# Optimization experiments

Measured on AMD Instinct MI355X. Metric: run time of the kernel, lower is better.

## Reference

```python
import jax, jax.numpy as jnp
import numpy as np

N, E = 100000, 1600000
IN, HID, HEADS, OUT = 128, 16, 8, 40
NEG_SLOPE = 0.2


def setup_inputs() -> dict:
    key = jax.random.key(0)
    ks = jax.random.split(key, 10)
    glorot = lambda k, shape, fan: (jax.random.normal(k, shape, jnp.float32) / np.float32(np.sqrt(fan)))
    return {
        "x": jax.random.normal(ks[0], (N, IN), jnp.float32),
        "edge_index": jax.random.randint(ks[1], (2, E), 0, N, dtype=jnp.int64),
        "W1": glorot(ks[2], (IN, HEADS * HID), IN),
        "att_src1": glorot(ks[3], (HEADS, HID), HID),
        "att_dst1": glorot(ks[4], (HEADS, HID), HID),
        "b1": jnp.zeros((HEADS * HID,), jnp.float32),
        "W2": glorot(ks[5], (HEADS * HID, OUT), HEADS * HID),
        "att_src2": glorot(ks[6], (1, OUT), OUT),
        "att_dst2": glorot(ks[7], (1, OUT), OUT),
        "b2": jnp.zeros((OUT,), jnp.float32),
    }


def gat_conv(x, W, a_src, a_dst, b, src, dst, n, heads, ch, concat):
    # x: [n, in], W: [in, heads*ch]
    h = (x @ W).reshape(n, heads, ch)                      # [n, H, C]
    e_s = jnp.einsum("nhc,hc->nh", h, a_src)               # per-node src logits
    e_d = jnp.einsum("nhc,hc->nh", h, a_dst)               # per-node dst logits
    alpha = jax.nn.leaky_relu(e_s[src] + e_d[dst], NEG_SLOPE)  # [E, H]
    # numerically stable softmax over incoming edges of each dst node
    m = jax.lax.stop_gradient(jax.ops.segment_max(alpha, dst, num_segments=n))
    ex = jnp.exp(alpha - m[dst])
    denom = jax.ops.segment_sum(ex, dst, num_segments=n)
    a = ex / (denom[dst] + 1e-16)                          # [E, H]
    out = jax.ops.segment_sum(h[src] * a[:, :, None], dst, num_segments=n)  # [n, H, C]
    out = out.reshape(n, heads * ch) if concat else out.mean(axis=1)
    return out + b


def reference(x, edge_index, W1, att_src1, att_dst1, b1, W2, att_src2, att_dst2, b2):
    n = x.shape[0]
    loops = jnp.arange(n, dtype=edge_index.dtype)
    src = jnp.concatenate([edge_index[0], loops])  # add_self_loops (PyG default)
    dst = jnp.concatenate([edge_index[1], loops])
    h1 = jax.nn.relu(gat_conv(x, W1, att_src1, att_dst1, b1, src, dst, n, HEADS, HID, True))
    # F.dropout(training=False) is identity in inference
    h2 = gat_conv(h1, W2, att_src2, att_dst2, b2, src, dst, n, 1, OUT, False)
    return jax.nn.log_softmax(h2, axis=1)
```

## Files before the change

### kernel.cpp

```cpp
#include <hip/hip_runtime.h>
#include <hip/hip_fp16.h>
#include <math.h>

#define NN 100000
#define EE 1600000
#define ET (EE + NN)
#define BWN 64
#define NBUCK 1563
#define ACHUNK 4096
#define NAB 416
#define MAXS 1792

typedef _Float16 f16x8 __attribute__((ext_vector_type(8)));
typedef float f32x4 __attribute__((ext_vector_type(4)));
typedef float f32x2 __attribute__((ext_vector_type(2)));

__device__ __forceinline__ float lrelu(float x) { return x > 0.f ? x : 0.2f * x; }

__global__ void k_w1pack(const float* __restrict__ W1, __half* __restrict__ w1p) {
    int idx = blockIdx.x * 256 + threadIdx.x;
    int j = idx & 7, lane = (idx >> 3) & 63, k0 = (idx >> 9) & 3;
    int ct = (idx >> 11) & 7, plane = idx >> 14;
    int k = k0 * 32 + (lane >> 4) * 8 + j;
    int c = ct * 16 + (lane & 15);
    float w = W1[k * 128 + c];
    _Float16 wh = (_Float16)w;
    _Float16 v = plane ? (_Float16)(w - (float)wh) : wh;
    w1p[idx] = *(__half*)&v;
}

__global__ __launch_bounds__(256) void k_gemm1(
        const float* __restrict__ x, const __half* __restrict__ w1p,
        const float* __restrict__ as1, const float* __restrict__ ad1,
        unsigned* __restrict__ h1b, float* __restrict__ es1, float* __restrict__ ed1) {
    int tid = threadIdx.x;
    int w = tid >> 6, lane = tid & 63;
    int rb = blockIdx.x * 64 + w * 16;
    int l15 = lane & 15, rg = lane >> 4;

    int arow = rb + l15;
    bool aok = arow < NN;
    const float4* x4 = (const float4*)x;
    f16x8 ah[4], ar[4];
    #pragma unroll
    for (int k0 = 0; k0 < 4; ++k0) {
        float4 p0 = make_float4(0.f, 0.f, 0.f, 0.f), p1 = p0;
        if (aok) {
            int fi = arow * 32 + k0 * 8 + rg * 2;
            p0 = x4[fi];
            p1 = x4[fi + 1];
        }
        float pv[8] = {p0.x, p0.y, p0.z, p0.w, p1.x, p1.y, p1.z, p1.w};
        #pragma unroll
        for (int j = 0; j < 8; ++j) {
            _Float16 h = (_Float16)pv[j];
            ah[k0][j] = h;
            ar[k0][j] = (_Float16)(pv[j] - (float)h);
        }
    }

    const f16x8* w1f = (const f16x8*)w1p;
    f32x4 acc[8];
    #pragma unroll
    for (int ct = 0; ct < 8; ++ct) acc[ct] = (f32x4){0.f, 0.f, 0.f, 0.f};
    #pragma unroll
    for (int ct = 0; ct < 8; ++ct) {
        #pragma unroll
        for (int k0 = 0; k0 < 4; ++k0) {
            f16x8 bh = w1f[(ct * 4 + k0) * 64 + lane];
            f16x8 br = w1f[2048 + (ct * 4 + k0) * 64 + lane];
            acc[ct] = __builtin_amdgcn_mfma_f32_16x16x32_f16(bh, ah[k0], acc[ct], 0, 0, 0);
            acc[ct] = __builtin_amdgcn_mfma_f32_16x16x32_f16(bh, ar[k0], acc[ct], 0, 0, 0);
            acc[ct] = __builtin_amdgcn_mfma_f32_16x16x32_f16(br, ah[k0], acc[ct], 0, 0, 0);
        }
    }

    int row = rb + l15;
    bool rok = row < NN;
    #pragma unroll
    for (int ct = 0; ct < 8; ++ct) {
        if (rok) {
            unsigned pw = __builtin_amdgcn_cvt_pk_fp8_f32(acc[ct][0], acc[ct][1], 0u, false);
            pw = __builtin_amdgcn_cvt_pk_fp8_f32(acc[ct][2], acc[ct][3], pw, true);
            h1b[row * 32 + ct * 4 + rg] = pw;
        }
        float4 a4 = ((const float4*)as1)[ct * 4 + rg];
        float4 d4 = ((const float4*)ad1)[ct * 4 + rg];
        float s = acc[ct][0] * a4.x + acc[ct][1] * a4.y + acc[ct][2] * a4.z + acc[ct][3] * a4.w;
        float d = acc[ct][0] * d4.x + acc[ct][1] * d4.y + acc[ct][2] * d4.z + acc[ct][3] * d4.w;
        s += __shfl_xor(s, 16); s += __shfl_xor(s, 32);
        d += __shfl_xor(d, 16); d += __shfl_xor(d, 32);
        if (rg == 0 && rok) { es1[row * 8 + ct] = s; ed1[row * 8 + ct] = d; }
    }
}

__global__ void k_bhist(const int* __restrict__ dst, int* __restrict__ bcnt) {
    __shared__ int lh[NBUCK];
    int t = threadIdx.x;
    for (int i = t; i < NBUCK; i += 256) lh[i] = 0;
    __syncthreads();
    int c0 = blockIdx.x * ACHUNK;
    #pragma unroll
    for (int i = 0; i < 16; ++i) {
        int e = c0 + t + i * 256;
        if (e < ET) {
            int d = (e < EE) ? dst[e] : e - EE;
            atomicAdd(&lh[d >> 6], 1);
        }
    }
    __syncthreads();
    for (int i = t; i < NBUCK; i += 256) {
        int c = lh[i];
        if (c) atomicAdd(&bcnt[i], c);
    }
}

__global__ void k_bscan(const int* __restrict__ bcnt, int* __restrict__ bbase,
                        int* __restrict__ bcur) {
    __shared__ int sd[256];
    int t = threadIdx.x;
    int base = t * 8;
    int v[8];
    int s = 0;
    #pragma unroll
    for (int j = 0; j < 8; ++j) {
        int i = base + j;
        v[j] = (i < NBUCK) ? bcnt[i] : 0;
        s += v[j];
    }
    sd[t] = s;
    __syncthreads();
    for (int off = 1; off < 256; off <<= 1) {
        int x = (t >= off) ? sd[t - off] : 0;
        __syncthreads();
        sd[t] += x;
        __syncthreads();
    }
    int excl = sd[t] - s;
    #pragma unroll
    for (int j = 0; j < 8; ++j) {
        int i = base + j;
        if (i <= NBUCK) { bbase[i] = excl; if (i < NBUCK) bcur[i] = excl; }
        excl += v[j];
    }
}

__global__ void k_bscatter(const int* __restrict__ src, const int* __restrict__ dst,
                           int* __restrict__ bcur, unsigned int* __restrict__ bedge) {
    __shared__ int lh[NBUCK];
    __shared__ int lb[NBUCK];
    int t = threadIdx.x;
    for (int i = t; i < NBUCK; i += 256) lh[i] = 0;
    __syncthreads();
    int c0 = blockIdx.x * ACHUNK;
    unsigned int val[16];
    int bkt[16];
    int rnk[16];
    #pragma unroll
    for (int i = 0; i < 16; ++i) {
        int e = c0 + t + i * 256;
        if (e < ET) {
            int s, d;
            if (e < EE) { s = src[e]; d = dst[e]; } else { s = d = e - EE; }
            int b = d >> 6;
            bkt[i] = b;
            val[i] = (unsigned)s | ((unsigned)(d & 63) << 24);
            rnk[i] = atomicAdd(&lh[b], 1);
        } else bkt[i] = -1;
    }
    __syncthreads();
    for (int i = t; i < NBUCK; i += 256) {
        int c = lh[i];
        lb[i] = c ? atomicAdd(&bcur[i], c) : 0;
    }
    __syncthreads();
    #pragma unroll
    for (int i = 0; i < 16; ++i)
        if (bkt[i] >= 0) bedge[lb[bkt[i]] + rnk[i]] = val[i];
}

__global__ void k_place(const unsigned int* __restrict__ bedge,
                        const int* __restrict__ bbase, int* __restrict__ rp,
                        int* __restrict__ col) {
    __shared__ int lh[BWN];
    __shared__ int ex[BWN + 1];
    __shared__ int lcur[BWN];
    __shared__ int stg[MAXS];
    int b = blockIdx.x, t = threadIdx.x;
    int beg = bbase[b], end = bbase[b + 1];
    if (t < BWN) { lh[t] = 0; lcur[t] = 0; }
    __syncthreads();
    for (int e = beg + t; e < end; e += 256) atomicAdd(&lh[(bedge[e] >> 24) & 63], 1);
    __syncthreads();
    if (t < 64) {
        int v = lh[t];
        int x = v;
        #pragma unroll
        for (int off = 1; off < 64; off <<= 1) {
            int y = __shfl_up(x, off);
            if (t >= off) x += y;
        }
        ex[t] = x - v;
        if (t == 63) ex[64] = x;
    }
    __syncthreads();
    int n = b * BWN + t;
    if (t < BWN && n < NN) rp[n] = beg + ex[t];
    if (b == 0 && t == 0) rp[NN] = ET;
    int S = ex[BWN];
    int lane = t & 63, w = t >> 6;
    if (S <= MAXS) {
        for (int e = beg + t; e < end; e += 256) {
            unsigned u = bedge[e];
            int i = (u >> 24) & 63;
            int pos = ex[i] + atomicAdd(&lcur[i], 1);
            stg[pos] = (int)(u & 0xFFFFFFu);
        }
        __syncthreads();
        for (int i = w; i < BWN; i += 4) {
            int sb = ex[i], d = lh[i];
            if (d <= 1) continue;
            if (d <= 64) {
                int vv = (lane < d) ? stg[sb + lane] : 0x7fffffff;
                #pragma unroll
                for (int k = 2; k <= 64; k <<= 1) {
                    #pragma unroll
                    for (int j = k >> 1; j > 0; j >>= 1) {
                        int other = __shfl_xor(vv, j);
                        bool lower = (lane & j) == 0;
                        bool up = (lane & k) == 0;
                        vv = (lower == up) ? min(vv, other) : max(vv, other);
                    }
                }
                if (lane < d) stg[sb + lane] = vv;
            } else if (lane == 0) {
                for (int p = sb + 1; p < sb + d; ++p) {
                    int key = stg[p]; int j = p - 1;
                    while (j >= sb && stg[j] > key) { stg[j + 1] = stg[j]; --j; }
                    stg[j + 1] = key;
                }
            }
        }
        __syncthreads();
        for (int j = t; j < S; j += 256) col[beg + j] = stg[j];
    } else {
        for (int e = beg + t; e < end; e += 256) {
            unsigned u = bedge[e];
            int i = (u >> 24) & 63;
            int pos = beg + ex[i] + atomicAdd(&lcur[i], 1);
            col[pos] = (int)(u & 0xFFFFFFu);
        }
        __syncthreads();
        if (t < BWN) {
            int sb = beg + ex[t], d = lh[t];
            for (int p = sb + 1; p < sb + d; ++p) {
                int key = col[p]; int j = p - 1;
                while (j >= sb && col[j] > key) { col[j + 1] = col[j]; --j; }
                col[j + 1] = key;
            }
        }
    }
}

__global__ void k_agg1(const int* __restrict__ rp, const int* __restrict__ col,
                       const uint4* __restrict__ h1v, const float* __restrict__ es1,
                       const float* __restrict__ ed1, const float* __restrict__ b1,
                       __half* __restrict__ out1h) {
    int gid = blockIdx.x * blockDim.x + threadIdx.x;
    int n = gid >> 3;
    int l = threadIdx.x & 7;
    if (n >= NN) return;
    float edn = ed1[n * 8 + l];
    int beg = rp[n], end = rp[n + 1];
    float acc[16];
    #pragma unroll
    for (int j = 0; j < 16; ++j) acc[j] = 0.f;
    float den = 0.f;
    int e = beg;
    int sA = col[e];
    int eB = (e + 1 < end) ? e + 1 : e;
    int sB = col[eB];
    float esA = es1[sA * 8 + l], esB = es1[sB * 8 + l];
    uint4 uA = h1v[sA * 8 + l];
    uint4 uB = h1v[sB * 8 + l];
    while (e < end) {
        int en = e + 2;
        int enA = (en < end) ? en : e;
        int enB = (en + 1 < end) ? en + 1 : enA;
        int nsA = col[enA], nsB = col[enB];
        float nesA = es1[nsA * 8 + l], nesB = es1[nsB * 8 + l];
        uint4 nuA = h1v[nsA * 8 + l];
        uint4 nuB = h1v[nsB * 8 + l];
        float exA = __expf(lrelu(esA + edn));
        float exB = (e + 1 < end) ? __expf(lrelu(esB + edn)) : 0.f;
        den += exA;
        den += exB;
        const unsigned* wA = (const unsigned*)&uA;
        const unsigned* wB = (const unsigned*)&uB;
        #pragma unroll
        for (int j = 0; j < 4; ++j) {
            f32x2 a01 = __builtin_amdgcn_cvt_pk_f32_fp8(wA[j], false);
            f32x2 a23 = __builtin_amdgcn_cvt_pk_f32_fp8(wA[j], true);
            f32x2 b01 = __builtin_amdgcn_cvt_pk_f32_fp8(wB[j], false);
            f32x2 b23 = __builtin_amdgcn_cvt_pk_f32_fp8(wB[j], true);
            acc[j * 4 + 0] += exA * a01.x; acc[j * 4 + 0] += exB * b01.x;
            acc[j * 4 + 1] += exA * a01.y; acc[j * 4 + 1] += exB * b01.y;
            acc[j * 4 + 2] += exA * a23.x; acc[j * 4 + 2] += exB * b23.x;
            acc[j * 4 + 3] += exA * a23.y; acc[j * 4 + 3] += exB * b23.y;
        }
        e = en;
        esA = nesA; esB = nesB;
        uA = nuA; uB = nuB;
    }
    float inv = 1.f / (den + 1e-16f);
    union { __half2 h[8]; uint4 u[2]; } cv;
    #pragma unroll
    for (int i = 0; i < 4; ++i) {
        float4 b = ((const float4*)b1)[l * 4 + i];
        float o0 = fmaxf(acc[i * 4]     * inv + b.x, 0.f);
        float o1 = fmaxf(acc[i * 4 + 1] * inv + b.y, 0.f);
        float o2 = fmaxf(acc[i * 4 + 2] * inv + b.z, 0.f);
        float o3 = fmaxf(acc[i * 4 + 3] * inv + b.w, 0.f);
        cv.h[i * 2]     = __floats2half2_rn(o0, o1);
        cv.h[i * 2 + 1] = __floats2half2_rn(o2, o3);
    }
    ((uint4*)out1h)[n * 16 + l * 2]     = cv.u[0];
    ((uint4*)out1h)[n * 16 + l * 2 + 1] = cv.u[1];
}

__global__ __launch_bounds__(256) void k_gemm2(
        const __half* __restrict__ out1h, const float* __restrict__ W2,
        const float* __restrict__ as2, const float* __restrict__ ad2,
        __half* __restrict__ h2h, float* __restrict__ es2, float* __restrict__ ed2) {
    __shared__ float xs[32][257];
    int tid = threadIdx.x;
    int rbase = blockIdx.x * 256;
    int row = rbase + tid;
    float acc[40];
    #pragma unroll
    for (int c = 0; c < 40; ++c) acc[c] = 0.f;
    for (int ch = 0; ch < 4; ++ch) {
        __syncthreads();
        #pragma unroll
        for (int i = 0; i < 4; ++i) {
            int idx = tid + i * 256;
            int r = idx >> 2, q = idx & 3;
            int rr = rbase + r;
            uint4 u = make_uint4(0, 0, 0, 0);
            if (rr < NN) u = ((const uint4*)out1h)[rr * 16 + ch * 4 + q];
            const __half2* hp = (const __half2*)&u;
            #pragma unroll
            for (int m = 0; m < 4; ++m) {
                float2 f = __half22float2(hp[m]);
                xs[q * 8 + m * 2][r] = f.x;
                xs[q * 8 + m * 2 + 1][r] = f.y;
            }
        }
        __syncthreads();
        #pragma unroll 4
        for (int j = 0; j < 32; ++j) {
            float xk = xs[j][tid];
            const float* wrow = W2 + (ch * 32 + j) * 40;
            #pragma unroll
            for (int c = 0; c < 40; ++c) acc[c] += xk * wrow[c];
        }
    }
    if (row < NN) {
        float s = 0.f, d = 0.f;
        #pragma unroll
        for (int c = 0; c < 40; ++c) { s += acc[c] * as2[c]; d += acc[c] * ad2[c]; }
        es2[row] = s;
        ed2[row] = d;
        union { __half2 h[20]; uint4 u[5]; } cv;
        #pragma unroll
        for (int c = 0; c < 20; ++c)
            cv.h[c] = __floats2half2_rn(acc[c * 2], acc[c * 2 + 1]);
        #pragma unroll
        for (int i = 0; i < 5; ++i) ((uint4*)h2h)[row * 5 + i] = cv.u[i];
    }
}

__global__ void k_agg2(const int* __restrict__ rp, const int* __restrict__ col,
                       const uint4* __restrict__ h2v, const float* __restrict__ es2,
                       const float* __restrict__ ed2, const float* __restrict__ b2,
                       float* __restrict__ out) {
    int gid = blockIdx.x * blockDim.x + threadIdx.x;
    int n = gid >> 3;
    int l = threadIdx.x & 7;
    if (n >= NN) return;
    bool qv = l < 5;
    float edn = ed2[n];
    int beg = rp[n], end = rp[n + 1];
    float acc[8];
    #pragma unroll
    for (int j = 0; j < 8; ++j) acc[j] = 0.f;
    float den = 0.f;
    int e = beg;
    int sA = col[e];
    int eB = (e + 1 < end) ? e + 1 : e;
    int sB = col[eB];
    float esA = es2[sA], esB = es2[sB];
    uint4 uA = qv ? h2v[sA * 5 + l] : make_uint4(0, 0, 0, 0);
    uint4 uB = qv ? h2v[sB * 5 + l] : make_uint4(0, 0, 0, 0);
    while (e < end) {
        int en = e + 2;
        int enA = (en < end) ? en : e;
        int enB = (en + 1 < end) ? en + 1 : enA;
        int nsA = col[enA], nsB = col[enB];
        float nesA = es2[nsA], nesB = es2[nsB];
        uint4 nuA = qv ? h2v[nsA * 5 + l] : make_uint4(0, 0, 0, 0);
        uint4 nuB = qv ? h2v[nsB * 5 + l] : make_uint4(0, 0, 0, 0);
        float exA = __expf(lrelu(esA + edn));
        float exB = (e + 1 < end) ? __expf(lrelu(esB + edn)) : 0.f;
        den += exA;
        den += exB;
        const __half2* pA = (const __half2*)&uA;
        const __half2* pB = (const __half2*)&uB;
        #pragma unroll
        for (int j = 0; j < 4; ++j) {
            float2 fA = __half22float2(pA[j]);
            float2 fB = __half22float2(pB[j]);
            acc[j * 2]     += exA * fA.x; acc[j * 2]     += exB * fB.x;
            acc[j * 2 + 1] += exA * fA.y; acc[j * 2 + 1] += exB * fB.y;
        }
        e = en;
        esA = nesA; esB = nesB;
        uA = nuA; uB = nuB;
    }
    float inv = 1.f / (den + 1e-16f);
    float v[8];
    float m = -INFINITY;
    if (qv) {
        #pragma unroll
        for (int j = 0; j < 8; ++j) {
            v[j] = acc[j] * inv + b2[l * 8 + j];
            m = fmaxf(m, v[j]);
        }
    }
    #pragma unroll
    for (int o = 1; o <= 4; o <<= 1) m = fmaxf(m, __shfl_xor(m, o));
    float es = 0.f;
    if (qv) {
        #pragma unroll
        for (int j = 0; j < 8; ++j) es += __expf(v[j] - m);
    }
    #pragma unroll
    for (int o = 1; o <= 4; o <<= 1) es += __shfl_xor(es, o);
    if (qv) {
        float ls = m + __logf(es);
        float4 o0, o1;
        o0.x = v[0] - ls; o0.y = v[1] - ls; o0.z = v[2] - ls; o0.w = v[3] - ls;
        o1.x = v[4] - ls; o1.y = v[5] - ls; o1.z = v[6] - ls; o1.w = v[7] - ls;
        ((float4*)out)[n * 10 + l * 2]     = o0;
        ((float4*)out)[n * 10 + l * 2 + 1] = o1;
    }
}

extern "C" void kernel_launch(void* const* d_in, const int* in_sizes, int n_in,
                              void* d_out, int out_size, void* d_ws, size_t ws_size,
                              hipStream_t stream) {
    const float* x   = (const float*)d_in[0];
    const int*   ei  = (const int*)d_in[1];
    const float* W1  = (const float*)d_in[2];
    const float* as1 = (const float*)d_in[3];
    const float* ad1 = (const float*)d_in[4];
    const float* b1  = (const float*)d_in[5];
    const float* W2  = (const float*)d_in[6];
    const float* as2 = (const float*)d_in[7];
    const float* ad2 = (const float*)d_in[8];
    const float* b2  = (const float*)d_in[9];
    float* out = (float*)d_out;

    const int* esrc = ei;
    const int* edst = ei + EE;

    unsigned* h1b = (unsigned*)d_ws;
    float* es1  = (float*)(h1b + NN * 32);
    float* ed1  = es1 + NN * 8;
    __half* out1h = (__half*)(ed1 + NN * 8);
    __half* h2h = out1h + NN * 128;
    float* es2  = (float*)(h2h + NN * 40);
    float* ed2  = es2 + NN;
    int* rp     = (int*)(ed2 + NN);
    int* col    = rp + NN + 1;
    int* bcnt   = col + ET;
    int* bbase  = bcnt + NBUCK;
    int* bcur   = bbase + NBUCK + 1;
    unsigned int* bedge = (unsigned int*)(bcur + NBUCK);
    __half* w1p = (__half*)(bedge + ET);

    hipMemsetAsync(bcnt, 0, NBUCK * sizeof(int), stream);
    k_bhist<<<NAB, 256, 0, stream>>>(edst, bcnt);
    k_bscan<<<1, 256, 0, stream>>>(bcnt, bbase, bcur);
    k_bscatter<<<NAB, 256, 0, stream>>>(esrc, edst, bcur, bedge);
    k_place<<<NBUCK, 256, 0, stream>>>(bedge, bbase, rp, col);

    k_w1pack<<<128, 256, 0, stream>>>(W1, w1p);
    k_gemm1<<<(NN + 63) / 64, 256, 0, stream>>>(x, w1p, as1, ad1, h1b, es1, ed1);
    k_agg1<<<(NN * 8 + 255) / 256, 256, 0, stream>>>(rp, col, (const uint4*)h1b, es1, ed1, b1, out1h);

    k_gemm2<<<(NN + 255) / 256, 256, 0, stream>>>(out1h, W2, as2, ad2, h2h, es2, ed2);
    k_agg2<<<(NN * 8 + 255) / 256, 256, 0, stream>>>(rp, col, (const uint4*)h2h, es2, ed2, b2, out);
}
```

Measured before the change: 279.2 us.

## Drop split-fp16 correction in GEMM1 and move GEMM2 onto fp16 MFMA

GEMM1 no longer splits x and W1 into high and residual fp16 parts, so it issues one MFMA per tile instead of three and loads only one weight plane. GEMM2 is rewritten from a scalar FMA loop over an LDS-transposed tile into 16x16x32 fp16 MFMAs, using a newly packed fp16 W2 zero-padded to 48 columns. The aim is to cut matrix-multiply compute and LDS traffic. The cost is lower accuracy, since all operands are now single fp16 with no error compensation.

Result: faster. 242.3 us (median of 2 runs) (-13.2%).

```diff
diff --git a/kernel.cpp b/kernel.cpp
--- a/kernel.cpp
+++ b/kernel.cpp
@@ -20,13 +20,21 @@
 __global__ void k_w1pack(const float* __restrict__ W1, __half* __restrict__ w1p) {
     int idx = blockIdx.x * 256 + threadIdx.x;
     int j = idx & 7, lane = (idx >> 3) & 63, k0 = (idx >> 9) & 3;
-    int ct = (idx >> 11) & 7, plane = idx >> 14;
+    int ct = (idx >> 11) & 7;
     int k = k0 * 32 + (lane >> 4) * 8 + j;
     int c = ct * 16 + (lane & 15);
-    float w = W1[k * 128 + c];
-    _Float16 wh = (_Float16)w;
-    _Float16 v = plane ? (_Float16)(w - (float)wh) : wh;
+    _Float16 v = (_Float16)W1[k * 128 + c];
     w1p[idx] = *(__half*)&v;
+}
+
+__global__ void k_w2pack(const float* __restrict__ W2, __half* __restrict__ w2p) {
+    int idx = blockIdx.x * 256 + threadIdx.x;
+    int j = idx & 7, lane = (idx >> 3) & 63, k0 = (idx >> 9) & 3;
+    int ct = idx >> 11;
+    int k = k0 * 32 + (lane >> 4) * 8 + j;
+    int c = ct * 16 + (lane & 15);
+    _Float16 v = (_Float16)((c < 40) ? W2[k * 40 + c] : 0.f);
+    w2p[idx] = *(__half*)&v;
 }
 
 __global__ __launch_bounds__(256) void k_gemm1(
@@ -41,7 +49,7 @@
     int arow = rb + l15;
     bool aok = arow < NN;
     const float4* x4 = (const float4*)x;
-    f16x8 ah[4], ar[4];
+    f16x8 ah[4];
     #pragma unroll
     for (int k0 = 0; k0 < 4; ++k0) {
         float4 p0 = make_float4(0.f, 0.f, 0.f, 0.f), p1 = p0;
@@ -52,11 +60,7 @@
         }
         float pv[8] = {p0.x, p0.y, p0.z, p0.w, p1.x, p1.y, p1.z, p1.w};
         #pragma unroll
-        for (int j = 0; j < 8; ++j) {
-            _Float16 h = (_Float16)pv[j];
-            ah[k0][j] = h;
-            ar[k0][j] = (_Float16)(pv[j] - (float)h);
-        }
+        for (int j = 0; j < 8; ++j) ah[k0][j] = (_Float16)pv[j];
     }
 
     const f16x8* w1f = (const f16x8*)w1p;
@@ -68,10 +72,7 @@
         #pragma unroll
         for (int k0 = 0; k0 < 4; ++k0) {
             f16x8 bh = w1f[(ct * 4 + k0) * 64 + lane];
-            f16x8 br = w1f[2048 + (ct * 4 + k0) * 64 + lane];
             acc[ct] = __builtin_amdgcn_mfma_f32_16x16x32_f16(bh, ah[k0], acc[ct], 0, 0, 0);
-            acc[ct] = __builtin_amdgcn_mfma_f32_16x16x32_f16(bh, ar[k0], acc[ct], 0, 0, 0);
-            acc[ct] = __builtin_amdgcn_mfma_f32_16x16x32_f16(br, ah[k0], acc[ct], 0, 0, 0);
         }
     }
 
@@ -329,55 +330,53 @@
 }
 
 __global__ __launch_bounds__(256) void k_gemm2(
-        const __half* __restrict__ out1h, const float* __restrict__ W2,
+        const __half* __restrict__ out1h, const __half* __restrict__ w2p,
         const float* __restrict__ as2, const float* __restrict__ ad2,
         __half* __restrict__ h2h, float* __restrict__ es2, float* __restrict__ ed2) {
-    __shared__ float xs[32][257];
     int tid = threadIdx.x;
-    int rbase = blockIdx.x * 256;
-    int row = rbase + tid;
-    float acc[40];
-    #pragma unroll
-    for (int c = 0; c < 40; ++c) acc[c] = 0.f;
-    for (int ch = 0; ch < 4; ++ch) {
-        __syncthreads();
-        #pragma unroll
-        for (int i = 0; i < 4; ++i) {
-            int idx = tid + i * 256;
-            int r = idx >> 2, q = idx & 3;
-            int rr = rbase + r;
-            uint4 u = make_uint4(0, 0, 0, 0);
-            if (rr < NN) u = ((const uint4*)out1h)[rr * 16 + ch * 4 + q];
-            const __half2* hp = (const __half2*)&u;
-            #pragma unroll
-            for (int m = 0; m < 4; ++m) {
-                float2 f = __half22float2(hp[m]);
-                xs[q * 8 + m * 2][r] = f.x;
-                xs[q * 8 + m * 2 + 1][r] = f.y;
+    int w = tid >> 6, lane = tid & 63;
+    int rb = blockIdx.x * 64 + w * 16;
+    int l15 = lane & 15, rg = lane >> 4;
+
+    int arow = rb + l15;
+    bool aok = arow < NN;
+    f16x8 af[4];
+    #pragma unroll
+    for (int k0 = 0; k0 < 4; ++k0) {
+        uint4 u = make_uint4(0, 0, 0, 0);
+        if (aok) u = ((const uint4*)out1h)[arow * 16 + k0 * 4 + rg];
+        af[k0] = *(f16x8*)&u;
+    }
+
+    const f16x8* w2f = (const f16x8*)w2p;
+    int row = rb + l15;
+    bool rok = row < NN;
+    float sacc = 0.f, dacc = 0.f;
+    #pragma unroll
+    for (int ct = 0; ct < 3; ++ct) {
+        f32x4 acc = (f32x4){0.f, 0.f, 0.f, 0.f};
+        #pragma unroll
+        for (int k0 = 0; k0 < 4; ++k0) {
+            f16x8 bh = w2f[(ct * 4 + k0) * 64 + lane];
+            acc = __builtin_amdgcn_mfma_f32_16x16x32_f16(bh, af[k0], acc, 0, 0, 0);
+        }
+        int cbase = ct * 16 + rg * 4;
+        if (cbase < 40) {
+            float4 a4 = ((const float4*)as2)[ct * 4 + rg];
+            float4 d4 = ((const float4*)ad2)[ct * 4 + rg];
+            sacc += acc[0] * a4.x + acc[1] * a4.y + acc[2] * a4.z + acc[3] * a4.w;
+            dacc += acc[0] * d4.x + acc[1] * d4.y + acc[2] * d4.z + acc[3] * d4.w;
+            if (rok) {
+                union { __half2 h[2]; uint2 u; } cv;
+                cv.h[0] = __floats2half2_rn(acc[0], acc[1]);
+                cv.h[1] = __floats2half2_rn(acc[2], acc[3]);
+                *(uint2*)&h2h[row * 40 + cbase] = cv.u;
             }
         }
-        __syncthreads();
-        #pragma unroll 4
-        for (int j = 0; j < 32; ++j) {
-            float xk = xs[j][tid];
-            const float* wrow = W2 + (ch * 32 + j) * 40;
-            #pragma unroll
-            for (int c = 0; c < 40; ++c) acc[c] += xk * wrow[c];
-        }
-    }
-    if (row < NN) {
-        float s = 0.f, d = 0.f;
-        #pragma unroll
-        for (int c = 0; c < 40; ++c) { s += acc[c] * as2[c]; d += acc[c] * ad2[c]; }
-        es2[row] = s;
-        ed2[row] = d;
-        union { __half2 h[20]; uint4 u[5]; } cv;
-        #pragma unroll
-        for (int c = 0; c < 20; ++c)
-            cv.h[c] = __floats2half2_rn(acc[c * 2], acc[c * 2 + 1]);
-        #pragma unroll
-        for (int i = 0; i < 5; ++i) ((uint4*)h2h)[row * 5 + i] = cv.u[i];
-    }
+    }
+    sacc += __shfl_xor(sacc, 16); sacc += __shfl_xor(sacc, 32);
+    dacc += __shfl_xor(dacc, 16); dacc += __shfl_xor(dacc, 32);
+    if (rg == 0 && rok) { es2[row] = sacc; ed2[row] = dacc; }
 }
 
 __global__ void k_agg2(const int* __restrict__ rp, const int* __restrict__ col,
@@ -488,6 +487,7 @@
     int* bcur   = bbase + NBUCK + 1;
     unsigned int* bedge = (unsigned int*)(bcur + NBUCK);
     __half* w1p = (__half*)(bedge + ET);
+    __half* w2p = w1p + 16384;
 
     hipMemsetAsync(bcnt, 0, NBUCK * sizeof(int), stream);
     k_bhist<<<NAB, 256, 0, stream>>>(edst, bcnt);
@@ -495,10 +495,11 @@
     k_bscatter<<<NAB, 256, 0, stream>>>(esrc, edst, bcur, bedge);
     k_place<<<NBUCK, 256, 0, stream>>>(bedge, bbase, rp, col);
 
-    k_w1pack<<<128, 256, 0, stream>>>(W1, w1p);
+    k_w1pack<<<64, 256, 0, stream>>>(W1, w1p);
     k_gemm1<<<(NN + 63) / 64, 256, 0, stream>>>(x, w1p, as1, ad1, h1b, es1, ed1);
     k_agg1<<<(NN * 8 + 255) / 256, 256, 0, stream>>>(rp, col, (const uint4*)h1b, es1, ed1, b1, out1h);
 
-    k_gemm2<<<(NN + 255) / 256, 256, 0, stream>>>(out1h, W2, as2, ad2, h2h, es2, ed2);
+    k_w2pack<<<24, 256, 0, stream>>>(W2, w2p);
+    k_gemm2<<<(NN + 63) / 64, 256, 0, stream>>>(out1h, w2p, as2, ad2, h2h, es2, ed2);
     k_agg2<<<(NN * 8 + 255) / 256, 256, 0, stream>>>(rp, col, (const uint4*)h2h, es2, ed2, b2, out);
 }
```
